# Kernel optimization log

Hardware: AMD Instinct MI355X
Metric: run time of the kernel (lower is better)

The kernel has to match this reference:

```python
import jax, jax.numpy as jnp
import numpy as np

H, FFN, E, TOPK = 1024, 4096, 8, 2
B, S = 2, 1024


def setup_inputs() -> dict:
    key = jax.random.key(0)
    k1, k2, k3, k4 = jax.random.split(key, 4)
    s_h = 1.0 / np.sqrt(H).astype(np.float32)
    s_f = 1.0 / np.sqrt(FFN).astype(np.float32)
    return {
        "hidden_states": jax.random.normal(k1, (B, S, H), jnp.float32),
        "gate_w": jax.random.normal(k2, (E, H), jnp.float32) * s_h,       # router Linear(H->E), no bias
        "w13": jax.random.normal(k3, (E, 2 * FFN, H), jnp.float32) * s_h,  # fused [w1; w3] per expert
        "w2": jax.random.normal(k4, (E, H, FFN), jnp.float32) * s_f,       # down-proj per expert
        "top_k": TOPK,
    }


def reference(hidden_states, gate_w, w13, w2, top_k):
    b, s, h = hidden_states.shape
    x = hidden_states.reshape(-1, h)                       # [T, H]
    router_logits = x @ gate_w.T                           # [T, E]
    rw = jax.nn.softmax(router_logits.astype(jnp.float32), axis=1)
    rw, sel = jax.lax.top_k(rw, top_k)                     # [T, K] each
    rw = rw / rw.sum(axis=-1, keepdims=True)
    rw = rw.astype(x.dtype)
    e_tot = gate_w.shape[0]
    f = w2.shape[2]
    # combine[t, e] = sum_k rw[t, k] * (sel[t, k] == e)
    combine = jnp.sum((sel[..., None] == jnp.arange(e_tot)) * rw[..., None], axis=1)  # [T, E]
    out = jnp.zeros_like(x)
    for e in range(e_tot):  # static small loop over experts
        g = x @ w13[e, :f].T            # [T, F] gate proj
        u = x @ w13[e, f:].T            # [T, F] up proj
        y = (jax.nn.silu(g) * u) @ w2[e].T  # [T, H]
        out = out + combine[:, e:e + 1] * y
    return out.reshape(b, s, h), router_logits
```

## Files before the change

### kernel.cpp

```cpp
#include <hip/hip_runtime.h>
#include <hip/hip_bf16.h>
#include <math.h>

#define H     1024
#define FFN   4096
#define NE    8
#define TOK   2048
#define PAIRS (TOK*2)
#define BM    128
#define BK    32
#define ROWCAP (PAIRS + NE*BM)
#define MAXTILES (ROWCAP/BM)

typedef unsigned short u16;
typedef __attribute__((ext_vector_type(8))) __bf16 bf16x8;
typedef __attribute__((ext_vector_type(4))) float  f32x4;

__device__ __forceinline__ unsigned cvt2(float a, float b) {
    __hip_bfloat162 h = __float22bfloat162_rn(float2{a, b});
    unsigned u;
    __builtin_memcpy(&u, &h, 4);
    return u;
}

#define GLD16(gp, lp) __builtin_amdgcn_global_load_lds( \
    (const __attribute__((address_space(1))) void*)(gp), \
    (__attribute__((address_space(3))) void*)(lp), 16, 0, 0)

__global__ __launch_bounds__(256) void k_cvtw(const float4* __restrict__ w13,
                                              const float4* __restrict__ w2,
                                              uint4* __restrict__ o13,
                                              uint4* __restrict__ o2) {
    size_t i = (size_t)blockIdx.x * 256 + threadIdx.x;
    const size_t N13 = (size_t)NE * 2 * FFN * H / 8;
    const float4* src; uint4* dst; size_t j;
    if (i < N13) { src = w13; dst = o13; j = i; }
    else         { src = w2;  dst = o2;  j = i - N13; }
    float4 a = src[2 * j], b = src[2 * j + 1];
    uint4 o = { cvt2(a.x, a.y), cvt2(a.z, a.w), cvt2(b.x, b.y), cvt2(b.z, b.w) };
    dst[j] = o;
}

__global__ void k_init(int* counts) {
    if (threadIdx.x < NE) counts[threadIdx.x] = 0;
}

__global__ void k_router(const float* __restrict__ x, const float* __restrict__ gw,
                         float* __restrict__ logits, int* counts,
                         int* __restrict__ sel, int* __restrict__ posn, float* __restrict__ wgt) {
    int lane = threadIdx.x & 63;
    int t = blockIdx.x * 4 + (threadIdx.x >> 6);
    float p[NE];
#pragma unroll
    for (int e = 0; e < NE; e++) p[e] = 0.f;
    for (int j = 0; j < H / 64; j++) {
        int h = lane + j * 64;
        float xv = x[(size_t)t * H + h];
#pragma unroll
        for (int e = 0; e < NE; e++) p[e] = fmaf(xv, gw[e * H + h], p[e]);
    }
#pragma unroll
    for (int off = 32; off; off >>= 1)
#pragma unroll
        for (int e = 0; e < NE; e++) p[e] += __shfl_xor(p[e], off, 64);
    if (lane == 0) {
        float mx = p[0];
#pragma unroll
        for (int e = 1; e < NE; e++) mx = fmaxf(mx, p[e]);
        float pe[NE];
#pragma unroll
        for (int e = 0; e < NE; e++) pe[e] = __expf(p[e] - mx);
        int i0 = 0;
#pragma unroll
        for (int e = 1; e < NE; e++) if (pe[e] > pe[i0]) i0 = e;
        int i1 = (i0 == 0) ? 1 : 0;
#pragma unroll
        for (int e = 0; e < NE; e++) if (e != i1 && e != i0 && pe[e] > pe[i1]) i1 = e;
        float w0 = pe[i0] / (pe[i0] + pe[i1]);
#pragma unroll
        for (int e = 0; e < NE; e++) logits[(size_t)t * NE + e] = p[e];
        int p0 = atomicAdd(&counts[i0], 1);
        int p1 = atomicAdd(&counts[i1], 1);
        sel[2 * t] = i0;  posn[2 * t] = p0;  wgt[2 * t] = w0;
        sel[2 * t + 1] = i1;  posn[2 * t + 1] = p1;  wgt[2 * t + 1] = 1.f - w0;
    }
}

__global__ void k_prefix(const int* __restrict__ counts, int* __restrict__ base,
                         int* __restrict__ tile_e) {
    if (threadIdx.x == 0) {
        int b = 0, tb = 0;
        for (int e = 0; e < NE; e++) {
            base[e] = b;
            int nt = (counts[e] + BM - 1) / BM;
            for (int i = 0; i < nt; i++) tile_e[tb++] = e;
            b += nt * BM;
        }
        base[NE] = b;
        while (tb < MAXTILES) tile_e[tb++] = -1;
    }
}

__global__ void k_gather(const float4* __restrict__ x4, const int* __restrict__ sel,
                         const int* __restrict__ posn, const int* __restrict__ base,
                         u16* __restrict__ xg) {
    int p = blockIdx.x;
    int lane = threadIdx.x;
    int t = p >> 1;
    int row = base[sel[p]] + posn[p];
#pragma unroll
    for (int i = 0; i < 4; i++) {
        int idx = i * 64 + lane;
        float4 v = x4[(size_t)t * (H / 4) + idx];
        uint2 o = { cvt2(v.x, v.y), cvt2(v.z, v.w) };
        *(uint2*)&xg[(size_t)row * H + idx * 4] = o;
    }
}

__global__ __launch_bounds__(256) void k_gemm1(const u16* __restrict__ xg,
                                               const u16* __restrict__ w13b,
                                               u16* __restrict__ act,
                                               const int* __restrict__ tile_e) {
    int e = tile_e[blockIdx.x];
    if (e < 0) return;
    __shared__ u16 As[BM * BK];
    __shared__ u16 Bs[BM * BK];

    int tid = threadIdx.x;
    int lane = tid & 63, wave = tid >> 6;
    int quad = lane >> 4, m16 = lane & 15;
    int wm = wave >> 1, wn = wave & 1;
    int row0 = blockIdx.x * BM;
    int n0 = blockIdx.y * 64;
    const u16* wb1 = w13b + ((size_t)e * 2 * FFN + n0) * H;
    const u16* wb3 = w13b + ((size_t)e * 2 * FFN + FFN + n0) * H;

    f32x4 accg[4][2], accu[4][2];
#pragma unroll
    for (int mi = 0; mi < 4; mi++)
#pragma unroll
        for (int ni = 0; ni < 2; ni++) { accg[mi][ni] = {0.f,0.f,0.f,0.f}; accu[mi][ni] = {0.f,0.f,0.f,0.f}; }

    int r4 = tid >> 2, c8 = (tid & 3) * 8;
    for (int kk = 0; kk < H; kk += BK) {
        GLD16(xg + (size_t)(row0 + r4) * H + kk + c8, As + tid * 8);
        GLD16(xg + (size_t)(row0 + 64 + r4) * H + kk + c8, As + 2048 + tid * 8);
        GLD16(wb1 + (size_t)r4 * H + kk + c8, Bs + tid * 8);
        GLD16(wb3 + (size_t)r4 * H + kk + c8, Bs + 2048 + tid * 8);
        __syncthreads();
        bf16x8 a[4], bg[2], bu[2];
#pragma unroll
        for (int mi = 0; mi < 4; mi++)
            a[mi] = *(const bf16x8*)&As[(wm * 64 + mi * 16 + m16) * BK + quad * 8];
#pragma unroll
        for (int ni = 0; ni < 2; ni++) {
            bg[ni] = *(const bf16x8*)&Bs[(wn * 32 + ni * 16 + m16) * BK + quad * 8];
            bu[ni] = *(const bf16x8*)&Bs[2048 + (wn * 32 + ni * 16 + m16) * BK + quad * 8];
        }
#pragma unroll
        for (int mi = 0; mi < 4; mi++)
#pragma unroll
            for (int ni = 0; ni < 2; ni++) {
                accg[mi][ni] = __builtin_amdgcn_mfma_f32_16x16x32_bf16(a[mi], bg[ni], accg[mi][ni], 0, 0, 0);
                accu[mi][ni] = __builtin_amdgcn_mfma_f32_16x16x32_bf16(a[mi], bu[ni], accu[mi][ni], 0, 0, 0);
            }
        __syncthreads();
    }
#pragma unroll
    for (int mi = 0; mi < 4; mi++)
#pragma unroll
        for (int ni = 0; ni < 2; ni++) {
            int gcol = n0 + wn * 32 + ni * 16 + m16;
            int grow = row0 + wm * 64 + mi * 16 + quad * 4;
#pragma unroll
            for (int r = 0; r < 4; r++) {
                float g = accg[mi][ni][r], u = accu[mi][ni][r];
                float hv = g * (1.f / (1.f + __expf(-g))) * u;
                unsigned pk = cvt2(hv, hv);
                act[(size_t)(grow + r) * FFN + gcol] = (u16)(pk & 0xffff);
            }
        }
}

__global__ __launch_bounds__(256) void k_gemm2(const u16* __restrict__ act,
                                               const u16* __restrict__ w2b,
                                               float* __restrict__ yc,
                                               const int* __restrict__ tile_e) {
    int e = tile_e[blockIdx.x];
    if (e < 0) return;
    __shared__ u16 As[BM * BK];
    __shared__ u16 Bs[BM * BK];

    int tid = threadIdx.x;
    int lane = tid & 63, wave = tid >> 6;
    int quad = lane >> 4, m16 = lane & 15;
    int wm = wave >> 1, wn = wave & 1;
    int row0 = blockIdx.x * BM;
    int n0 = blockIdx.y * 128;
    int k0 = blockIdx.z * (FFN / 2);
    const u16* wb = w2b + ((size_t)e * H + n0) * FFN;
    float* ycp = yc + (size_t)blockIdx.z * ROWCAP * H;

    f32x4 acc[4][4];
#pragma unroll
    for (int mi = 0; mi < 4; mi++)
#pragma unroll
        for (int ni = 0; ni < 4; ni++) acc[mi][ni] = {0.f,0.f,0.f,0.f};

    int r4 = tid >> 2, c8 = (tid & 3) * 8;
    for (int kk = k0; kk < k0 + FFN / 2; kk += BK) {
        GLD16(act + (size_t)(row0 + r4) * FFN + kk + c8, As + tid * 8);
        GLD16(act + (size_t)(row0 + 64 + r4) * FFN + kk + c8, As + 2048 + tid * 8);
        GLD16(wb + (size_t)r4 * FFN + kk + c8, Bs + tid * 8);
        GLD16(wb + (size_t)(64 + r4) * FFN + kk + c8, Bs + 2048 + tid * 8);
        __syncthreads();
        bf16x8 a[4], b[4];
#pragma unroll
        for (int mi = 0; mi < 4; mi++)
            a[mi] = *(const bf16x8*)&As[(wm * 64 + mi * 16 + m16) * BK + quad * 8];
#pragma unroll
        for (int ni = 0; ni < 4; ni++)
            b[ni] = *(const bf16x8*)&Bs[(wn * 64 + ni * 16 + m16) * BK + quad * 8];
#pragma unroll
        for (int mi = 0; mi < 4; mi++)
#pragma unroll
            for (int ni = 0; ni < 4; ni++)
                acc[mi][ni] = __builtin_amdgcn_mfma_f32_16x16x32_bf16(a[mi], b[ni], acc[mi][ni], 0, 0, 0);
        __syncthreads();
    }
#pragma unroll
    for (int mi = 0; mi < 4; mi++)
#pragma unroll
        for (int ni = 0; ni < 4; ni++)
#pragma unroll
            for (int r = 0; r < 4; r++) {
                int grow = row0 + wm * 64 + mi * 16 + quad * 4 + r;
                int gcol = n0 + wn * 64 + ni * 16 + m16;
                ycp[(size_t)grow * H + gcol] = acc[mi][ni][r];
            }
}

__global__ void k_combine(const float4* __restrict__ yc4, const int* __restrict__ sel,
                          const int* __restrict__ posn, const int* __restrict__ base,
                          const float* __restrict__ wgt, float4* __restrict__ out4) {
    int t = blockIdx.x;
    int j = threadIdx.x;
    int r0 = base[sel[2 * t]] + posn[2 * t];
    int r1 = base[sel[2 * t + 1]] + posn[2 * t + 1];
    float w0 = wgt[2 * t], w1 = wgt[2 * t + 1];
    const size_t P = (size_t)ROWCAP * (H / 4);
    float4 a0 = yc4[(size_t)r0 * (H / 4) + j];
    float4 a1 = yc4[(size_t)r0 * (H / 4) + j + P];
    float4 b0 = yc4[(size_t)r1 * (H / 4) + j];
    float4 b1 = yc4[(size_t)r1 * (H / 4) + j + P];
    float4 o = { w0 * (a0.x + a1.x) + w1 * (b0.x + b1.x),
                 w0 * (a0.y + a1.y) + w1 * (b0.y + b1.y),
                 w0 * (a0.z + a1.z) + w1 * (b0.z + b1.z),
                 w0 * (a0.w + a1.w) + w1 * (b0.w + b1.w) };
    out4[(size_t)t * (H / 4) + j] = o;
}

extern "C" void kernel_launch(void* const* d_in, const int* in_sizes, int n_in,
                              void* d_out, int out_size, void* d_ws, size_t ws_size,
                              hipStream_t stream) {
    const float* x   = (const float*)d_in[0];
    const float* gw  = (const float*)d_in[1];
    const float* w13 = (const float*)d_in[2];
    const float* w2  = (const float*)d_in[3];
    float* out    = (float*)d_out;
    float* logits = out + (size_t)TOK * H;

    char* ws = (char*)d_ws;
    int*   counts = (int*)ws;
    int*   base   = (int*)(ws + 256);
    int*   tile_e = (int*)(ws + 512);
    int*   sel    = (int*)(ws + 1024);
    int*   posn   = (int*)(ws + 1024 + 4 * PAIRS);
    float* wgt    = (float*)(ws + 1024 + 8 * PAIRS);
    u16*   xg     = (u16*)(ws + 65536);
    u16*   act    = xg + (size_t)ROWCAP * H;
    u16*   w13b   = act + (size_t)ROWCAP * FFN;
    u16*   w2b    = w13b + (size_t)NE * 2 * FFN * H;
    float* yc     = (float*)w13b;

    k_cvtw<<<49152, 256, 0, stream>>>((const float4*)w13, (const float4*)w2,
                                      (uint4*)w13b, (uint4*)w2b);
    k_init<<<1, 64, 0, stream>>>(counts);
    k_router<<<TOK / 4, 256, 0, stream>>>(x, gw, logits, counts, sel, posn, wgt);
    k_prefix<<<1, 64, 0, stream>>>(counts, base, tile_e);
    k_gather<<<PAIRS, 64, 0, stream>>>((const float4*)x, sel, posn, base, xg);
    dim3 g1(MAXTILES, FFN / 64);
    k_gemm1<<<g1, 256, 0, stream>>>(xg, w13b, act, tile_e);
    dim3 g2(MAXTILES, H / 128, 2);
    k_gemm2<<<g2, 256, 0, stream>>>(act, w2b, yc, tile_e);
    k_combine<<<TOK, 256, 0, stream>>>((const float4*)yc, sel, posn, base, wgt, (float4*)out);
}
```

Measured before the change: 758.1 us.

## Store GEMM LDS tiles in MFMA fragment order and raise gemm2 split-K to four

Both grouped GEMMs now load A and B tiles into LDS in the order the MFMA fragments are read, so each lane reads a contiguous 16 bytes instead of row-strided addresses. This is meant to remove LDS bank conflicts on fragment reads. gemm2 split-K goes from 2 to 4 to launch more blocks, and the partial-sum buffer moves to its own workspace region instead of aliasing w13b. The combine kernel reads and reduces four partials, which costs extra fp32 traffic and more workspace.

```diff
diff --git a/kernel.cpp b/kernel.cpp
--- a/kernel.cpp
+++ b/kernel.cpp
@@ -11,6 +11,7 @@
 #define BK    32
 #define ROWCAP (PAIRS + NE*BM)
 #define MAXTILES (ROWCAP/BM)
+#define SPLITK 4
 
 typedef unsigned short u16;
 typedef __attribute__((ext_vector_type(8))) __bf16 bf16x8;
@@ -123,8 +124,9 @@
                                                const int* __restrict__ tile_e) {
     int e = tile_e[blockIdx.x];
     if (e < 0) return;
-    __shared__ u16 As[BM * BK];
-    __shared__ u16 Bs[BM * BK];
+    __shared__ alignas(16) u16 As[4096];
+    __shared__ alignas(16) u16 Bg[2048];
+    __shared__ alignas(16) u16 Bu[2048];
 
     int tid = threadIdx.x;
     int lane = tid & 63, wave = tid >> 6;
@@ -132,6 +134,7 @@
     int wm = wave >> 1, wn = wave & 1;
     int row0 = blockIdx.x * BM;
     int n0 = blockIdx.y * 64;
+    const u16* xb  = xg + (size_t)row0 * H;
     const u16* wb1 = w13b + ((size_t)e * 2 * FFN + n0) * H;
     const u16* wb3 = w13b + ((size_t)e * 2 * FFN + FFN + n0) * H;
 
@@ -141,21 +144,24 @@
 #pragma unroll
         for (int ni = 0; ni < 2; ni++) { accg[mi][ni] = {0.f,0.f,0.f,0.f}; accu[mi][ni] = {0.f,0.f,0.f,0.f}; }
 
-    int r4 = tid >> 2, c8 = (tid & 3) * 8;
+    int ar = ((tid >> 6) & 3) * 16 + (tid & 15);
+    int ak = ((tid >> 4) & 3) * 8;
+    int br = (tid >> 7) * 32 + ((tid >> 6) & 1) * 16 + (tid & 15);
+
     for (int kk = 0; kk < H; kk += BK) {
-        GLD16(xg + (size_t)(row0 + r4) * H + kk + c8, As + tid * 8);
-        GLD16(xg + (size_t)(row0 + 64 + r4) * H + kk + c8, As + 2048 + tid * 8);
-        GLD16(wb1 + (size_t)r4 * H + kk + c8, Bs + tid * 8);
-        GLD16(wb3 + (size_t)r4 * H + kk + c8, Bs + 2048 + tid * 8);
+        GLD16(xb + (size_t)ar * H + kk + ak, As + tid * 8);
+        GLD16(xb + (size_t)(ar + 64) * H + kk + ak, As + 2048 + tid * 8);
+        GLD16(wb1 + (size_t)br * H + kk + ak, Bg + tid * 8);
+        GLD16(wb3 + (size_t)br * H + kk + ak, Bu + tid * 8);
         __syncthreads();
         bf16x8 a[4], bg[2], bu[2];
 #pragma unroll
         for (int mi = 0; mi < 4; mi++)
-            a[mi] = *(const bf16x8*)&As[(wm * 64 + mi * 16 + m16) * BK + quad * 8];
+            a[mi] = *(const bf16x8*)&As[(wm * 256 + mi * 64 + lane) * 8];
 #pragma unroll
         for (int ni = 0; ni < 2; ni++) {
-            bg[ni] = *(const bf16x8*)&Bs[(wn * 32 + ni * 16 + m16) * BK + quad * 8];
-            bu[ni] = *(const bf16x8*)&Bs[2048 + (wn * 32 + ni * 16 + m16) * BK + quad * 8];
+            bg[ni] = *(const bf16x8*)&Bg[(wn * 128 + ni * 64 + lane) * 8];
+            bu[ni] = *(const bf16x8*)&Bu[(wn * 128 + ni * 64 + lane) * 8];
         }
 #pragma unroll
         for (int mi = 0; mi < 4; mi++)
@@ -188,8 +194,8 @@
                                                const int* __restrict__ tile_e) {
     int e = tile_e[blockIdx.x];
     if (e < 0) return;
-    __shared__ u16 As[BM * BK];
-    __shared__ u16 Bs[BM * BK];
+    __shared__ alignas(16) u16 As[4096];
+    __shared__ alignas(16) u16 Bs[4096];
 
     int tid = threadIdx.x;
     int lane = tid & 63, wave = tid >> 6;
@@ -197,7 +203,8 @@
     int wm = wave >> 1, wn = wave & 1;
     int row0 = blockIdx.x * BM;
     int n0 = blockIdx.y * 128;
-    int k0 = blockIdx.z * (FFN / 2);
+    int k0 = blockIdx.z * (FFN / SPLITK);
+    const u16* ab = act + (size_t)row0 * FFN;
     const u16* wb = w2b + ((size_t)e * H + n0) * FFN;
     float* ycp = yc + (size_t)blockIdx.z * ROWCAP * H;
 
@@ -207,20 +214,22 @@
 #pragma unroll
         for (int ni = 0; ni < 4; ni++) acc[mi][ni] = {0.f,0.f,0.f,0.f};
 
-    int r4 = tid >> 2, c8 = (tid & 3) * 8;
-    for (int kk = k0; kk < k0 + FFN / 2; kk += BK) {
-        GLD16(act + (size_t)(row0 + r4) * FFN + kk + c8, As + tid * 8);
-        GLD16(act + (size_t)(row0 + 64 + r4) * FFN + kk + c8, As + 2048 + tid * 8);
-        GLD16(wb + (size_t)r4 * FFN + kk + c8, Bs + tid * 8);
-        GLD16(wb + (size_t)(64 + r4) * FFN + kk + c8, Bs + 2048 + tid * 8);
+    int ar = ((tid >> 6) & 3) * 16 + (tid & 15);
+    int ak = ((tid >> 4) & 3) * 8;
+
+    for (int kk = k0; kk < k0 + FFN / SPLITK; kk += BK) {
+        GLD16(ab + (size_t)ar * FFN + kk + ak, As + tid * 8);
+        GLD16(ab + (size_t)(ar + 64) * FFN + kk + ak, As + 2048 + tid * 8);
+        GLD16(wb + (size_t)ar * FFN + kk + ak, Bs + tid * 8);
+        GLD16(wb + (size_t)(ar + 64) * FFN + kk + ak, Bs + 2048 + tid * 8);
         __syncthreads();
         bf16x8 a[4], b[4];
 #pragma unroll
         for (int mi = 0; mi < 4; mi++)
-            a[mi] = *(const bf16x8*)&As[(wm * 64 + mi * 16 + m16) * BK + quad * 8];
+            a[mi] = *(const bf16x8*)&As[(wm * 256 + mi * 64 + lane) * 8];
 #pragma unroll
         for (int ni = 0; ni < 4; ni++)
-            b[ni] = *(const bf16x8*)&Bs[(wn * 64 + ni * 16 + m16) * BK + quad * 8];
+            b[ni] = *(const bf16x8*)&Bs[(wn * 256 + ni * 64 + lane) * 8];
 #pragma unroll
         for (int mi = 0; mi < 4; mi++)
 #pragma unroll
@@ -249,14 +258,16 @@
     int r1 = base[sel[2 * t + 1]] + posn[2 * t + 1];
     float w0 = wgt[2 * t], w1 = wgt[2 * t + 1];
     const size_t P = (size_t)ROWCAP * (H / 4);
-    float4 a0 = yc4[(size_t)r0 * (H / 4) + j];
-    float4 a1 = yc4[(size_t)r0 * (H / 4) + j + P];
-    float4 b0 = yc4[(size_t)r1 * (H / 4) + j];
-    float4 b1 = yc4[(size_t)r1 * (H / 4) + j + P];
-    float4 o = { w0 * (a0.x + a1.x) + w1 * (b0.x + b1.x),
-                 w0 * (a0.y + a1.y) + w1 * (b0.y + b1.y),
-                 w0 * (a0.z + a1.z) + w1 * (b0.z + b1.z),
-                 w0 * (a0.w + a1.w) + w1 * (b0.w + b1.w) };
+    float4 o = {0.f, 0.f, 0.f, 0.f};
+#pragma unroll
+    for (int z = 0; z < SPLITK; z++) {
+        float4 a = yc4[(size_t)r0 * (H / 4) + j + z * P];
+        float4 b = yc4[(size_t)r1 * (H / 4) + j + z * P];
+        o.x += w0 * a.x + w1 * b.x;
+        o.y += w0 * a.y + w1 * b.y;
+        o.z += w0 * a.z + w1 * b.z;
+        o.w += w0 * a.w + w1 * b.w;
+    }
     out4[(size_t)t * (H / 4) + j] = o;
 }
 
@@ -277,11 +288,11 @@
     int*   sel    = (int*)(ws + 1024);
     int*   posn   = (int*)(ws + 1024 + 4 * PAIRS);
     float* wgt    = (float*)(ws + 1024 + 8 * PAIRS);
-    u16*   xg     = (u16*)(ws + 65536);
+    u16*   xg     = (u16*)(ws + 131072);
     u16*   act    = xg + (size_t)ROWCAP * H;
     u16*   w13b   = act + (size_t)ROWCAP * FFN;
     u16*   w2b    = w13b + (size_t)NE * 2 * FFN * H;
-    float* yc     = (float*)w13b;
+    float* yc     = (float*)(w2b + (size_t)NE * H * FFN);
 
     k_cvtw<<<49152, 256, 0, stream>>>((const float4*)w13, (const float4*)w2,
                                       (uint4*)w13b, (uint4*)w2b);
@@ -291,7 +302,7 @@
     k_gather<<<PAIRS, 64, 0, stream>>>((const float4*)x, sel, posn, base, xg);
     dim3 g1(MAXTILES, FFN / 64);
     k_gemm1<<<g1, 256, 0, stream>>>(xg, w13b, act, tile_e);
-    dim3 g2(MAXTILES, H / 128, 2);
+    dim3 g2(MAXTILES, H / 128, SPLITK);
     k_gemm2<<<g2, 256, 0, stream>>>(act, w2b, yc, tile_e);
     k_combine<<<TOK, 256, 0, stream>>>((const float4*)yc, sel, posn, base, wgt, (float4*)out);
 }
```

New measurement: 823.8 us. 8.7% more time.
